# Performance work log

Measured on AMD Instinct MI355X. Metric: run time of the kernel, lower is better.

## Reference

```python
import jax, jax.numpy as jnp
import numpy as np

EMBED_DIM = 768
NUM_HEADS = 12
HEAD_DIM = EMBED_DIM // NUM_HEADS  # 64


def setup_inputs() -> dict:
    key = jax.random.key(0)
    ks = jax.random.split(key, 8)
    B, T, C, H, D = 32, 512, EMBED_DIM, NUM_HEADS, HEAD_DIM
    s = 0.02
    x = jax.random.normal(ks[0], (B, T, C), dtype=jnp.float32)
    # per-head qkv: Linear(C -> 3D) stacked over heads
    Wqkv = jax.random.normal(ks[1], (H, C, 3 * D), dtype=jnp.float32) * s
    bqkv = jax.random.normal(ks[2], (H, 3 * D), dtype=jnp.float32) * s
    # per-head output proj: Linear(D -> C) stacked over heads
    Wph = jax.random.normal(ks[3], (H, D, C), dtype=jnp.float32) * s
    bph = jax.random.normal(ks[4], (H, C), dtype=jnp.float32) * s
    # final proj: Linear(H*C -> C)  (H*C == num_heads*num_heads*head_dim)
    Wproj = jax.random.normal(ks[5], (H * C, C), dtype=jnp.float32) * s
    bproj = jax.random.normal(ks[6], (C,), dtype=jnp.float32) * s
    return {"x": x, "Wqkv": Wqkv, "bqkv": bqkv, "Wph": Wph, "bph": bph,
            "Wproj": Wproj, "bproj": bproj}


def reference(x, Wqkv, bqkv, Wph, bph, Wproj, bproj):
    B, T, C = x.shape
    H, D = NUM_HEADS, HEAD_DIM
    scale = 1.0 / np.sqrt(D).astype(np.float32)
    # batched per-head qkv projection: [B,H,T,3D]
    qkv = jnp.einsum('btc,hcd->bhtd', x, Wqkv) + bqkv[None, :, None, :]
    q, k, v = jnp.split(qkv, 3, axis=-1)  # each [B,H,T,D]
    attn = jnp.einsum('bhtd,bhsd->bhts', q, k) * scale
    sa_probs = jax.nn.softmax(attn, axis=-1)  # [B,H,T,T]
    sa = jnp.einsum('bhts,bhsd->bhtd', sa_probs, v)  # [B,H,T,D]
    # per-head projection D -> C, then concat over heads (head-major order)
    heads_out = jnp.einsum('bhtd,hdc->bhtc', sa, Wph) + bph[None, :, None, :]
    cat = heads_out.transpose(0, 2, 1, 3).reshape(B, T, H * C)
    sa_out = cat @ Wproj + bproj  # [B,T,C]
    return sa_out, sa_probs
```

## Files before the change

kernel.cpp:

```cpp
#include <hip/hip_runtime.h>
#include <stdint.h>

typedef float f32x4 __attribute__((ext_vector_type(4)));
typedef short bf16x8 __attribute__((ext_vector_type(8)));

__device__ __forceinline__ unsigned short f2bf(float f) {
  union { float f; uint32_t u; } v; v.f = f;
  uint32_t r = v.u + 0x7FFFu + ((v.u >> 16) & 1u);
  return (unsigned short)(r >> 16);
}

__global__ __launch_bounds__(256) void conv_f2b(const float* __restrict__ in,
                                                unsigned short* __restrict__ out, long n) {
  long i = ((long)blockIdx.x * 256 + threadIdx.x) * 4;
  if (i + 3 < n) {
    float4 f = *(const float4*)(in + i);
    ushort4 o;
    o.x = f2bf(f.x); o.y = f2bf(f.y); o.z = f2bf(f.z); o.w = f2bf(f.w);
    *(ushort4*)(out + i) = o;
  }
}

__global__ __launch_bounds__(256) void transpose_f2b(const float* __restrict__ in,
                                                     unsigned short* __restrict__ out,
                                                     int R, int C) {
  __shared__ unsigned short tile[32][33];
  long base = (long)blockIdx.z * R * C;
  in += base; out += base;
  int c0 = blockIdx.x * 32, r0 = blockIdx.y * 32;
  int tx = threadIdx.x & 31, ty = threadIdx.x >> 5;
#pragma unroll
  for (int i = 0; i < 32; i += 8)
    tile[ty + i][tx] = f2bf(in[(long)(r0 + ty + i) * C + c0 + tx]);
  __syncthreads();
#pragma unroll
  for (int i = 0; i < 32; i += 8)
    out[(long)(c0 + ty + i) * R + r0 + tx] = tile[tx][ty + i];
}

__global__ __launch_bounds__(256) void bias_fuse(const float* __restrict__ bph,
                                                 const float* __restrict__ Wproj,
                                                 const float* __restrict__ bproj,
                                                 float* __restrict__ bfused) {
  int j = blockIdx.x * 256 + threadIdx.x;
  int r0 = blockIdx.y * 256;
  float acc = 0.f;
  for (int r = r0; r < r0 + 256; r++)
    acc += bph[r] * Wproj[(long)r * 768 + j];
  if (blockIdx.y == 0) acc += bproj[j];
  atomicAdd(&bfused[j], acc);
}

__device__ __forceinline__ void stage8(const unsigned short* __restrict__ g,
                                       unsigned short* __restrict__ s) {
  *(uint4*)s = *(const uint4*)g;
}

template <typename AT, typename Epi>
__global__ __launch_bounds__(256) void gemm_bt(const AT* __restrict__ A, long asb, int lda,
                                               const unsigned short* __restrict__ Bt, long bsb,
                                               int ldb, int K, Epi epi) {
  __shared__ __align__(16) unsigned short As[64][32];
  __shared__ __align__(16) unsigned short Bs[64][32];
  const int tid = threadIdx.x;
  const int row = tid >> 2;
  const int kc = (tid & 3) * 8;
  const int lane = tid & 63;
  const int w = tid >> 6;
  const int quad = lane >> 4, lr = lane & 15;
  const int bz = blockIdx.z;

  f32x4 acc[4];
#pragma unroll
  for (int i = 0; i < 4; i++) acc[i] = (f32x4){0.f, 0.f, 0.f, 0.f};

  const AT* Ab = A + (long)bz * asb + (long)(blockIdx.y * 64 + row) * lda;
  const unsigned short* Bb = Bt + (long)bz * bsb + (long)(blockIdx.x * 64 + row) * ldb;

  for (int k0 = 0; k0 < K; k0 += 32) {
    stage8(Ab + k0 + kc, &As[row][kc]);
    stage8(Bb + k0 + kc, &Bs[row][kc]);
    __syncthreads();
    bf16x8 a = *(const bf16x8*)&As[w * 16 + lr][quad * 8];
#pragma unroll
    for (int nt = 0; nt < 4; nt++) {
      bf16x8 b = *(const bf16x8*)&Bs[nt * 16 + lr][quad * 8];
      acc[nt] = __builtin_amdgcn_mfma_f32_16x16x32_bf16(a, b, acc[nt], 0, 0, 0);
    }
    __syncthreads();
  }
  const int mg = blockIdx.y * 64 + w * 16 + quad * 4;
  const int ng = blockIdx.x * 64 + lr;
#pragma unroll
  for (int nt = 0; nt < 4; nt++)
#pragma unroll
    for (int r = 0; r < 4; r++)
      epi(bz, mg + r, ng + nt * 16, acc[nt][r]);
}

struct EpiQKV {
  const float* bqkv;
  unsigned short *q, *k, *vt;
  __device__ void operator()(int, int m, int n, float val) const {
    int h = n / 192, d3 = n - h * 192;
    unsigned short bv = f2bf(val + bqkv[n]);
    int b = m >> 9, t = m & 511;
    long bh = b * 12 + h;
    if (d3 < 64)        q[(bh * 512 + t) * 64 + d3] = bv;
    else if (d3 < 128)  k[(bh * 512 + t) * 64 + (d3 - 64)] = bv;
    else                vt[(bh * 64 + (d3 - 128)) * 512 + t] = bv;
  }
};
struct EpiWf {
  unsigned short* wft;
  __device__ void operator()(int z, int m, int n, float val) const {
    wft[(long)n * 768 + z * 64 + m] = f2bf(val);
  }
};
struct EpiOut {
  float* out;
  const float* bfused;
  __device__ void operator()(int, int m, int n, float val) const {
    out[(long)m * 768 + n] = val + bfused[n];
  }
};

__global__ __launch_bounds__(256, 2) void attn_fused(
    const unsigned short* __restrict__ q,
    const unsigned short* __restrict__ k,
    const unsigned short* __restrict__ vt,
    float* __restrict__ probs,
    unsigned short* __restrict__ sa)
{
  __shared__ __align__(16) unsigned short P[64][512];
  const int tid = threadIdx.x;
  const int w = tid >> 6;
  const int lane = tid & 63;
  const int quad = lane >> 4, lr = lane & 15;
  const int bh = blockIdx.y;
  const int q0 = blockIdx.x * 64;

  const unsigned short* Qb = q + ((long)bh * 512 + q0 + w * 16) * 64;
  const unsigned short* Kb = k + (long)bh * 512 * 64;
  const unsigned short* Vb = vt + (long)bh * 64 * 512;

  bf16x8 a0 = *(const bf16x8*)(Qb + (long)lr * 64 + quad * 8);
  bf16x8 a1 = *(const bf16x8*)(Qb + (long)lr * 64 + quad * 8 + 32);
  f32x4 acc[32];
#pragma unroll
  for (int nt = 0; nt < 32; nt++) acc[nt] = (f32x4){0.f, 0.f, 0.f, 0.f};
#pragma unroll
  for (int nt = 0; nt < 32; nt++) {
    const unsigned short* kr = Kb + (long)(nt * 16 + lr) * 64 + quad * 8;
    bf16x8 b0 = *(const bf16x8*)kr;
    bf16x8 b1 = *(const bf16x8*)(kr + 32);
    acc[nt] = __builtin_amdgcn_mfma_f32_16x16x32_bf16(a0, b0, acc[nt], 0, 0, 0);
    acc[nt] = __builtin_amdgcn_mfma_f32_16x16x32_bf16(a1, b1, acc[nt], 0, 0, 0);
  }

  float mx[4], sum[4];
#pragma unroll
  for (int r = 0; r < 4; r++) {
    float m = -1e30f;
#pragma unroll
    for (int nt = 0; nt < 32; nt++) m = fmaxf(m, acc[nt][r]);
#pragma unroll
    for (int off = 8; off; off >>= 1) m = fmaxf(m, __shfl_xor(m, off, 64));
    mx[r] = m;
    sum[r] = 0.f;
  }
#pragma unroll
  for (int nt = 0; nt < 32; nt++)
#pragma unroll
    for (int r = 0; r < 4; r++) {
      float p = __expf(0.125f * (acc[nt][r] - mx[r]));
      acc[nt][r] = p;
      sum[r] += p;
    }
#pragma unroll
  for (int r = 0; r < 4; r++) {
    float s = sum[r];
#pragma unroll
    for (int off = 8; off; off >>= 1) s += __shfl_xor(s, off, 64);
    sum[r] = 1.0f / s;
  }
  float* Pr = probs + ((long)bh * 512 + q0 + w * 16 + quad * 4) * 512 + lr;
  const int mbase = w * 16 + quad * 4;
#pragma unroll
  for (int nt = 0; nt < 32; nt++)
#pragma unroll
    for (int r = 0; r < 4; r++) {
      float p = acc[nt][r] * sum[r];
      Pr[(long)r * 512 + nt * 16] = p;
      int m = mbase + r;
      int byte = m * 1024 + (((lr + nt * 16) * 2) ^ (((m ^ (m >> 3)) & 7) << 4));
      *(unsigned short*)((char*)P + byte) = f2bf(p);
    }
  __syncthreads();

  f32x4 o[4];
#pragma unroll
  for (int dt = 0; dt < 4; dt++) o[dt] = (f32x4){0.f, 0.f, 0.f, 0.f};
  const int mrow = w * 16 + lr;
  const int swz = ((mrow ^ (mrow >> 3)) & 7) << 4;
#pragma unroll
  for (int ks = 0; ks < 16; ks++) {
    bf16x8 pa = *(const bf16x8*)((char*)P + mrow * 1024 + ((quad * 16 + ks * 64) ^ swz));
#pragma unroll
    for (int dt = 0; dt < 4; dt++) {
      bf16x8 vb = *(const bf16x8*)(Vb + (long)(dt * 16 + lr) * 512 + quad * 8 + ks * 32);
      o[dt] = __builtin_amdgcn_mfma_f32_16x16x32_bf16(pa, vb, o[dt], 0, 0, 0);
    }
  }
  const int b = bh / 12, h = bh - b * 12;
  unsigned short* So = sa + ((long)(b * 512 + q0 + w * 16 + quad * 4)) * 768 + h * 64;
#pragma unroll
  for (int dt = 0; dt < 4; dt++)
#pragma unroll
    for (int r = 0; r < 4; r++)
      So[(long)r * 768 + dt * 16 + lr] = f2bf(o[dt][r]);
}

extern "C" void kernel_launch(void* const* d_in, const int* in_sizes, int n_in,
                              void* d_out, int out_size, void* d_ws, size_t ws_size,
                              hipStream_t stream) {
  const float* x     = (const float*)d_in[0];
  const float* Wqkv  = (const float*)d_in[1];
  const float* bqkv  = (const float*)d_in[2];
  const float* Wph   = (const float*)d_in[3];
  const float* bph   = (const float*)d_in[4];
  const float* Wproj = (const float*)d_in[5];
  const float* bproj = (const float*)d_in[6];
  float* out = (float*)d_out;
  float* probs = out + 12582912L;

  char* ws = (char*)d_ws;
  auto alloc = [&](size_t bytes) {
    char* p = ws;
    ws += (bytes + 255) & ~(size_t)255;
    return p;
  };
  unsigned short* x_b    = (unsigned short*)alloc(16384L * 768 * 2);
  unsigned short* wqkvt  = (unsigned short*)alloc(2304L * 768 * 2);
  unsigned short* wph_b  = (unsigned short*)alloc(768L * 768 * 2);
  unsigned short* wprojt = (unsigned short*)alloc(768L * 9216 * 2);
  unsigned short* wft    = (unsigned short*)alloc(768L * 768 * 2);
  float*          bfused = (float*)alloc(768 * 4);
  unsigned short* qb     = (unsigned short*)alloc(12582912L * 2);
  unsigned short* kb     = (unsigned short*)alloc(12582912L * 2);
  unsigned short* vtb    = (unsigned short*)alloc(12582912L * 2);
  unsigned short* sa     = (unsigned short*)alloc(12582912L * 2);

  hipMemsetAsync(bfused, 0, 768 * 4, stream);

  conv_f2b<<<12288, 256, 0, stream>>>(x, x_b, 12582912L);
  conv_f2b<<<576, 256, 0, stream>>>(Wph, wph_b, 589824L);
  transpose_f2b<<<dim3(6, 24, 12), 256, 0, stream>>>(Wqkv, wqkvt, 768, 192);
  transpose_f2b<<<dim3(24, 288, 1), 256, 0, stream>>>(Wproj, wprojt, 9216, 768);
  bias_fuse<<<dim3(3, 36), 256, 0, stream>>>(bph, Wproj, bproj, bfused);

  gemm_bt<<<dim3(36, 256, 1), 256, 0, stream>>>(x_b, 0L, 768, wqkvt, 0L, 768, 768,
                                                EpiQKV{bqkv, qb, kb, vtb});
  attn_fused<<<dim3(8, 384), 256, 0, stream>>>(qb, kb, vtb, probs, sa);
  gemm_bt<<<dim3(12, 1, 12), 256, 0, stream>>>(wph_b, 49152L, 768, wprojt, 768L, 9216, 768,
                                               EpiWf{wft});
  gemm_bt<<<dim3(12, 256, 1), 256, 0, stream>>>(sa, 0L, 768, wft, 0L, 768, 768,
                                                EpiOut{out, bfused});
}
```

Baseline: 958.8 us.

## Add 128x128 tiled bf16 MFMA GEMM with direct global-to-LDS loads

Adds a gemm128 kernel in which each 256-thread block computes a 128x128 output tile. Each wave holds a 4x4 grid of 16x16 MFMA accumulators, and operands are staged through global_load_lds so they go straight from global memory to LDS without passing through registers. The QKV projection and the final output GEMM now use this kernel instead of the 64x64 gemm_bt. The larger tile is meant to raise operand reuse and cut global and LDS traffic per FLOP. In exchange it uses more accumulator registers, launches fewer blocks, and there is still no double buffering between loads and MFMAs.

```diff
diff --git a/kernel.cpp b/kernel.cpp
--- a/kernel.cpp
+++ b/kernel.cpp
@@ -8,6 +8,12 @@
   union { float f; uint32_t u; } v; v.f = f;
   uint32_t r = v.u + 0x7FFFu + ((v.u >> 16) & 1u);
   return (unsigned short)(r >> 16);
+}
+
+__device__ __forceinline__ void gload16(const unsigned short* g, unsigned short* l) {
+  __builtin_amdgcn_global_load_lds(
+      (const __attribute__((address_space(1))) void*)g,
+      (__attribute__((address_space(3))) void*)l, 16, 0, 0);
 }
 
 __global__ __launch_bounds__(256) void conv_f2b(const float* __restrict__ in,
@@ -96,6 +102,62 @@
 #pragma unroll
     for (int r = 0; r < 4; r++)
       epi(bz, mg + r, ng + nt * 16, acc[nt][r]);
+}
+
+template <typename Epi>
+__global__ __launch_bounds__(256) void gemm128(const unsigned short* __restrict__ A, int lda,
+                                               const unsigned short* __restrict__ Bt, int ldb,
+                                               int K, Epi epi) {
+  __shared__ __align__(16) unsigned short As[128][32];
+  __shared__ __align__(16) unsigned short Bs[128][32];
+  const int tid = threadIdx.x;
+  const int lane = tid & 63;
+  const int w = tid >> 6;
+  const int quad = lane >> 4, lr = lane & 15;
+  const int sr = lane >> 2;
+  const int sc = (lane & 3) * 8;
+
+  f32x4 acc[4][4];
+#pragma unroll
+  for (int i = 0; i < 4; i++)
+#pragma unroll
+    for (int j = 0; j < 4; j++) acc[i][j] = (f32x4){0.f, 0.f, 0.f, 0.f};
+
+  const unsigned short* Ag = A + (long)(blockIdx.y * 128 + w * 16 + sr) * lda + sc;
+  const unsigned short* Bg = Bt + (long)(blockIdx.x * 128 + w * 16 + sr) * ldb + sc;
+  unsigned short* Al0 = &As[w * 16][0];
+  unsigned short* Al1 = &As[64 + w * 16][0];
+  unsigned short* Bl0 = &Bs[w * 16][0];
+  unsigned short* Bl1 = &Bs[64 + w * 16][0];
+  const int wr = (w >> 1) * 64, wc = (w & 1) * 64;
+
+  for (int k0 = 0; k0 < K; k0 += 32) {
+    gload16(Ag + k0, Al0);
+    gload16(Ag + k0 + (long)64 * lda, Al1);
+    gload16(Bg + k0, Bl0);
+    gload16(Bg + k0 + (long)64 * ldb, Bl1);
+    __syncthreads();
+    bf16x8 a[4], b[4];
+#pragma unroll
+    for (int mt = 0; mt < 4; mt++) a[mt] = *(const bf16x8*)&As[wr + mt * 16 + lr][quad * 8];
+#pragma unroll
+    for (int nt = 0; nt < 4; nt++) b[nt] = *(const bf16x8*)&Bs[wc + nt * 16 + lr][quad * 8];
+#pragma unroll
+    for (int mt = 0; mt < 4; mt++)
+#pragma unroll
+      for (int nt = 0; nt < 4; nt++)
+        acc[mt][nt] = __builtin_amdgcn_mfma_f32_16x16x32_bf16(a[mt], b[nt], acc[mt][nt], 0, 0, 0);
+    __syncthreads();
+  }
+  const int mg0 = blockIdx.y * 128 + wr + quad * 4;
+  const int ng0 = blockIdx.x * 128 + wc + lr;
+#pragma unroll
+  for (int mt = 0; mt < 4; mt++)
+#pragma unroll
+    for (int nt = 0; nt < 4; nt++)
+#pragma unroll
+      for (int r = 0; r < 4; r++)
+        epi(0, mg0 + mt * 16 + r, ng0 + nt * 16, acc[mt][nt][r]);
 }
 
 struct EpiQKV {
@@ -259,11 +321,11 @@
   transpose_f2b<<<dim3(24, 288, 1), 256, 0, stream>>>(Wproj, wprojt, 9216, 768);
   bias_fuse<<<dim3(3, 36), 256, 0, stream>>>(bph, Wproj, bproj, bfused);
 
-  gemm_bt<<<dim3(36, 256, 1), 256, 0, stream>>>(x_b, 0L, 768, wqkvt, 0L, 768, 768,
-                                                EpiQKV{bqkv, qb, kb, vtb});
+  gemm128<<<dim3(18, 128), 256, 0, stream>>>(x_b, 768, wqkvt, 768, 768,
+                                             EpiQKV{bqkv, qb, kb, vtb});
   attn_fused<<<dim3(8, 384), 256, 0, stream>>>(qb, kb, vtb, probs, sa);
   gemm_bt<<<dim3(12, 1, 12), 256, 0, stream>>>(wph_b, 49152L, 768, wprojt, 768L, 9216, 768,
                                                EpiWf{wft});
-  gemm_bt<<<dim3(12, 256, 1), 256, 0, stream>>>(sa, 0L, 768, wft, 0L, 768, 768,
-                                                EpiOut{out, bfused});
-}
+  gemm128<<<dim3(6, 128), 256, 0, stream>>>(sa, 768, wft, 768, 768,
+                                            EpiOut{out, bfused});
+}
```

After: 901.6 us. 6.0% less time.
